# Optimization experiments

Hardware: AMD Instinct MI355X
Metric: run time of the kernel (lower is better)

## Reference

```python
import jax, jax.numpy as jnp
import numpy as np

B, T, D, H = 32, 2048, 256, 256  # batch, length, input_size, hidden_size


def _lstm_layer(x, W_ih, W_hh, b, reverse):
    """Single-direction LSTM over time. x: [B,T,Din]; W_ih: [4H,Din]; W_hh: [4H,H]; b: [4H].
    Gate order: i, f, g, o (PyTorch convention). Returns hidden states [B,T,H]."""
    # Precompute input contribution for all timesteps in one big GEMM.
    xg = jnp.einsum('btd,gd->btg', x, W_ih) + b  # [B,T,4H]
    Hh = W_hh.shape[1]
    Bb = x.shape[0]

    def step(carry, xg_t):
        h, c = carry
        g = xg_t + h @ W_hh.T  # [B,4H]
        i, f, gc, o = jnp.split(g, 4, axis=-1)
        c = jax.nn.sigmoid(f) * c + jax.nn.sigmoid(i) * jnp.tanh(gc)
        h = jax.nn.sigmoid(o) * jnp.tanh(c)
        return (h, c), h

    init = (jnp.zeros((Bb, Hh), x.dtype), jnp.zeros((Bb, Hh), x.dtype))
    _, hs = jax.lax.scan(step, init, jnp.swapaxes(xg, 0, 1), reverse=reverse)  # [T,B,H]
    return jnp.swapaxes(hs, 0, 1)  # [B,T,H]


def setup_inputs() -> dict:
    key = jax.random.key(0)
    ks = jax.random.split(key, 13)
    s = 0.05
    G = 4 * H
    inp = {
        'x': jax.random.normal(ks[0], (B, T, D), dtype=jnp.float32),
        # layer 0 (input size D), forward and reverse directions
        'W_ih_f0': jax.random.normal(ks[1], (G, D), dtype=jnp.float32) * s,
        'W_hh_f0': jax.random.normal(ks[2], (G, H), dtype=jnp.float32) * s,
        'b_f0': jnp.zeros((G,), dtype=jnp.float32),
        'W_ih_r0': jax.random.normal(ks[3], (G, D), dtype=jnp.float32) * s,
        'W_hh_r0': jax.random.normal(ks[4], (G, H), dtype=jnp.float32) * s,
        'b_r0': jnp.zeros((G,), dtype=jnp.float32),
        # layer 1 (input size 2H because bidirectional)
        'W_ih_f1': jax.random.normal(ks[5], (G, 2 * H), dtype=jnp.float32) * s,
        'W_hh_f1': jax.random.normal(ks[6], (G, H), dtype=jnp.float32) * s,
        'b_f1': jnp.zeros((G,), dtype=jnp.float32),
        'W_ih_r1': jax.random.normal(ks[7], (G, 2 * H), dtype=jnp.float32) * s,
        'W_hh_r1': jax.random.normal(ks[8], (G, H), dtype=jnp.float32) * s,
        'b_r1': jnp.zeros((G,), dtype=jnp.float32),
    }
    return inp


def reference(x, W_ih_f0, W_hh_f0, b_f0, W_ih_r0, W_hh_r0, b_r0,
              W_ih_f1, W_hh_f1, b_f1, W_ih_r1, W_hh_r1, b_r1):
    # Layer 0: bidirectional over raw input
    h0 = jnp.concatenate([
        _lstm_layer(x, W_ih_f0, W_hh_f0, b_f0, reverse=False),
        _lstm_layer(x, W_ih_r0, W_hh_r0, b_r0, reverse=True),
    ], axis=-1)  # [B,T,2H]
    # Layer 1: bidirectional over concatenated hidden states
    h1 = jnp.concatenate([
        _lstm_layer(h0, W_ih_f1, W_hh_f1, b_f1, reverse=False),
        _lstm_layer(h0, W_ih_r1, W_hh_r1, b_r1, reverse=True),
    ], axis=-1)  # [B,T,2H]
    return h1
```

## Files before the change

kernel.cpp:

```cpp
#include <hip/hip_runtime.h>
#include <stdint.h>


#define Bn 32
#define Tn 2048
#define Hn 256

#define L2E 1.4426950408889634f
#define L2E2 2.8853900817779268f
#define L2E4 5.7707801635558535f

typedef short short8 __attribute__((ext_vector_type(8)));
typedef float f32x4 __attribute__((ext_vector_type(4)));
typedef unsigned int u32x4 __attribute__((ext_vector_type(4)));

extern "C" __device__ float __ocml_native_exp2_f32(float);

__device__ inline unsigned short f2b(float f) {
  union { float f; unsigned u; } v; v.f = f;
  unsigned r = v.u + 0x7fffu + ((v.u >> 16) & 1u);
  return (unsigned short)(r >> 16);
}
__device__ inline float asf(unsigned u) {
  union { unsigned u; float f; } v; v.u = u; return v.f;
}
__device__ inline float sig2(float x) {
  return __builtin_amdgcn_rcpf(1.f + __ocml_native_exp2_f32(-x));
}

template <int K, bool AF32>
__global__ __launch_bounds__(256, 2) void xg_gemm(
    const void* __restrict__ Ain,
    const float* __restrict__ Wf, const float* __restrict__ bf_,
    const float* __restrict__ Wr, const float* __restrict__ br_,
    unsigned short* __restrict__ xg) {
  constexpr int KI = K / 32;
  const int bid = blockIdx.x;
  const int scan = bid & 1;
  const int sgrp = (bid >> 1) & 7;
  const int mchunk = bid >> 4;
  const int wave = threadIdx.x >> 6;
  const int lane = threadIdx.x & 63;
  const int l15 = lane & 15, quad = lane >> 4;
  const int stripe = sgrp * 4 + wave;
  const int gi0 = stripe * 32;
  const int wp = stripe & 7;
  const int gg = stripe >> 3;

  const float* W = scan ? Wr : Wf;
  const float* bias = scan ? br_ : bf_;
  const float gscale = (gg == 2) ? L2E2 : L2E;

  short8 bfr[KI][2];
  float bias2[2];
#pragma unroll
  for (int sub = 0; sub < 2; ++sub) {
    const int gi = gi0 + sub * 16 + l15;
    bias2[sub] = bias[gi] * gscale;
#pragma unroll
    for (int ki = 0; ki < KI; ++ki) {
      const float* src = W + (size_t)gi * K + ki * 32 + quad * 8;
      short8 v;
#pragma unroll
      for (int j = 0; j < 8; ++j) v[j] = (short)f2b(src[j] * gscale);
      bfr[ki][sub] = v;
    }
  }

  const size_t scanoff = (size_t)scan << 26;
#pragma unroll 1
  for (int mt0 = 0; mt0 < 16; ++mt0) {
    const int mt = mchunk * 16 + mt0;
    const size_t row = (size_t)mt * 16 + l15;
    f32x4 acc[2];
#pragma unroll
    for (int sub = 0; sub < 2; ++sub) {
      f32x4 bi = {bias2[sub], bias2[sub], bias2[sub], bias2[sub]};
      acc[sub] = bi;
    }
#pragma unroll
    for (int ki = 0; ki < KI; ++ki) {
      short8 af;
      if constexpr (AF32) {
        const float* ap = (const float*)Ain + row * K + ki * 32 + quad * 8;
        f32x4 a0 = *(const f32x4*)ap;
        f32x4 a1 = *(const f32x4*)(ap + 4);
#pragma unroll
        for (int j = 0; j < 4; ++j) { af[j] = (short)f2b(a0[j]); af[4 + j] = (short)f2b(a1[j]); }
      } else {
        const unsigned short* ap = (const unsigned short*)Ain + row * K + ki * 32 + quad * 8;
        af = *(const short8*)ap;
      }
#pragma unroll
      for (int sub = 0; sub < 2; ++sub)
        acc[sub] = __builtin_amdgcn_mfma_f32_16x16x32_bf16(af, bfr[ki][sub], acc[sub], 0, 0, 0);
    }
#pragma unroll
    for (int sub = 0; sub < 2; ++sub) {
#pragma unroll
      for (int r = 0; r < 4; ++r) {
        const int orow = mt * 16 + quad * 4 + r;
        const int m = orow >> 11, t = orow & 2047;
        size_t idx = scanoff
          + ((((size_t)t * 2 + (m >> 4)) * 8 + wp) << 11)
          + ((size_t)((((m >> 2) & 3) << 4) + l15) << 5)
          + (sub << 4) + (gg << 2) + (m & 3);
        xg[idx] = f2b(acc[sub][r]);
      }
    }
  }
}

template <bool LAYER1>
__global__ __launch_bounds__(512, 2) void lstm_scan(
    const unsigned short* __restrict__ xg,
    const float* __restrict__ Whh_f, const float* __restrict__ Whh_r,
    unsigned short* __restrict__ h0out,
    float* __restrict__ dout) {
  __shared__ __align__(16) char smem[131072 + 2 * 8192];

  const int bid = blockIdx.x;
  const int scan = bid & 1;
  const int mh = bid >> 1;
  const int wave = threadIdx.x >> 6;
  const int lane = threadIdx.x & 63;
  const int l15 = lane & 15, quad = lane >> 4;

  const float* Whh = scan ? Whh_r : Whh_f;

  short8 wres[2][3][8];
#pragma unroll
  for (int uh = 0; uh < 2; ++uh)
#pragma unroll
    for (int g = 0; g < 3; ++g) {
      const float ws = (g == 2) ? L2E2 : L2E;
#pragma unroll
      for (int ki = 0; ki < 8; ++ki) {
        const int col = g * 256 + wave * 32 + uh * 16 + l15;
        const float* src = Whh + ((size_t)col << 8) + ki * 32 + quad * 8;
        f32x4 a0 = *(const f32x4*)src;
        f32x4 a1 = *(const f32x4*)(src + 4);
        short8 v;
#pragma unroll
        for (int j = 0; j < 4; ++j) { v[j] = (short)f2b(a0[j] * ws); v[4 + j] = (short)f2b(a1[j] * ws); }
        wres[uh][g][ki] = v;
      }
    }
#pragma unroll
  for (int uh = 0; uh < 2; ++uh)
#pragma unroll
    for (int ki = 0; ki < 8; ++ki) {
      const int col = 768 + wave * 32 + uh * 16 + l15;
      const float* src = Whh + ((size_t)col << 8) + ki * 32 + quad * 8;
      f32x4 a0 = *(const f32x4*)src;
      f32x4 a1 = *(const f32x4*)(src + 4);
      short8 v;
#pragma unroll
      for (int j = 0; j < 4; ++j) { v[j] = (short)f2b(a0[j] * L2E); v[4 + j] = (short)f2b(a1[j] * L2E); }
      *(short8*)(smem + ((((wave << 1) + uh) << 3) + ki) * 1024 + lane * 16) = v;
    }

  const size_t scanoff = (size_t)scan << 26;
  const int tstep = scan ? -1 : 1;
  const int t0 = scan ? (Tn - 1) : 0;
  const size_t lane_off = (size_t)lane * 32;
  u32x4 xr[2][2];
  {
    const unsigned short* xb =
        xg + scanoff + ((((size_t)t0 * 2 + mh) * 8 + wave) << 11) + lane_off;
    xr[0][0] = *(const u32x4*)(xb + 0);
    xr[0][1] = *(const u32x4*)(xb + 8);
    xr[1][0] = *(const u32x4*)(xb + 16);
    xr[1][1] = *(const u32x4*)(xb + 24);
  }

  char* hbuf = smem + 131072;
  float c_st[2][4] = {{0.f, 0.f, 0.f, 0.f}, {0.f, 0.f, 0.f, 0.f}};

  __syncthreads();

#pragma unroll 1
  for (int s = 0; s < Tn; ++s) {
    const int t = scan ? (Tn - 1 - s) : s;
    const int tn = (s < Tn - 1) ? (t + tstep) : t;
    const unsigned short* xbn =
        xg + scanoff + ((((size_t)tn * 2 + mh) * 8 + wave) << 11) + lane_off;
    const int p_r = (s - 1) & 1, p_w = s & 1;

#pragma unroll
    for (int uh = 0; uh < 2; ++uh) {
      f32x4 acc[4];
#pragma unroll
      for (int g = 0; g < 4; ++g) {
        unsigned lo = xr[uh][g >> 1][2 * (g & 1)];
        unsigned hi = xr[uh][g >> 1][2 * (g & 1) + 1];
        acc[g][0] = asf(lo << 16); acc[g][1] = asf(lo & 0xffff0000u);
        acc[g][2] = asf(hi << 16); acc[g][3] = asf(hi & 0xffff0000u);
      }
      if (uh == 1) {
        xr[0][0] = *(const u32x4*)(xbn + 0);
        xr[0][1] = *(const u32x4*)(xbn + 8);
      }

      if (s > 0) {
        const char* hr = hbuf + p_r * 8192 + lane * 16;
        const char* wl0 = smem + (((wave << 1) + uh) << 13) + lane * 16;
#pragma unroll
        for (int ki = 0; ki < 8; ++ki) {
          short8 a = *(const short8*)(hr + (ki << 10));
          short8 wl = *(const short8*)(wl0 + (ki << 10));
          acc[0] = __builtin_amdgcn_mfma_f32_16x16x32_bf16(a, wres[uh][0][ki], acc[0], 0, 0, 0);
          acc[1] = __builtin_amdgcn_mfma_f32_16x16x32_bf16(a, wres[uh][1][ki], acc[1], 0, 0, 0);
          acc[2] = __builtin_amdgcn_mfma_f32_16x16x32_bf16(a, wres[uh][2][ki], acc[2], 0, 0, 0);
          acc[3] = __builtin_amdgcn_mfma_f32_16x16x32_bf16(a, wl,              acc[3], 0, 0, 0);
        }
      }

      const int ubase = wave * 32 + uh * 16 + l15;
      char* hwb = hbuf + p_w * 8192 + wave * 1024 +
                  ((uh * 2 + (l15 >> 3)) << 8) + (l15 & 7) * 2;
#pragma unroll
      for (int r = 0; r < 4; ++r) {
        float ig = sig2(acc[0][r]);
        float fg = sig2(acc[1][r]);
        float gt = __builtin_fmaf(sig2(acc[2][r]), L2E4, -L2E2);
        float og = sig2(acc[3][r]);
        float cv = __builtin_fmaf(fg, c_st[uh][r], ig * gt);
        c_st[uh][r] = cv;
        float hv = og * __builtin_fmaf(sig2(cv), 2.f, -1.f);
        unsigned short h16 = f2b(hv);
        int pk = __shfl_xor((int)h16, 1);
        const int row = quad * 4 + r;
        if (!(lane & 1)) {
          unsigned pv = (unsigned)h16 | ((unsigned)pk << 16);
          *(unsigned*)(hwb + row * 16) = pv;
        }
        const int b = mh * 16 + row;
        if constexpr (!LAYER1) {
          h0out[(((size_t)b * Tn + t) << 9) + scan * Hn + ubase] = h16;
        } else {
          dout[(((size_t)b * Tn + t) << 9) + scan * Hn + ubase] = hv;
        }
      }

      if (uh == 1) {
        xr[1][0] = *(const u32x4*)(xbn + 16);
        xr[1][1] = *(const u32x4*)(xbn + 24);
      }
    }

    __syncthreads();
  }
}

extern "C" void kernel_launch(void* const* d_in, const int* in_sizes, int n_in,
                              void* d_out, int out_size, void* d_ws, size_t ws_size,
                              hipStream_t stream) {
  (void)in_sizes; (void)n_in; (void)out_size; (void)ws_size;
  const float* x      = (const float*)d_in[0];
  const float* Wih_f0 = (const float*)d_in[1];
  const float* Whh_f0 = (const float*)d_in[2];
  const float* b_f0   = (const float*)d_in[3];
  const float* Wih_r0 = (const float*)d_in[4];
  const float* Whh_r0 = (const float*)d_in[5];
  const float* b_r0   = (const float*)d_in[6];
  const float* Wih_f1 = (const float*)d_in[7];
  const float* Whh_f1 = (const float*)d_in[8];
  const float* b_f1   = (const float*)d_in[9];
  const float* Wih_r1 = (const float*)d_in[10];
  const float* Whh_r1 = (const float*)d_in[11];
  const float* b_r1   = (const float*)d_in[12];

  char* ws = (char*)d_ws;
  unsigned short* xgbuf = (unsigned short*)ws;
  size_t off = (size_t)2 * Tn * Bn * 1024 * sizeof(unsigned short);
  unsigned short* h0out = (unsigned short*)(ws + off);

  dim3 blkA(256), blkB(512);
  xg_gemm<256, true><<<dim3(4096), blkA, 0, stream>>>(
      (const void*)x, Wih_f0, b_f0, Wih_r0, b_r0, xgbuf);
  lstm_scan<false><<<dim3(4), blkB, 0, stream>>>(
      xgbuf, Whh_f0, Whh_r0, h0out, (float*)nullptr);
  xg_gemm<512, false><<<dim3(4096), blkA, 0, stream>>>(
      (const void*)h0out, Wih_f1, b_f1, Wih_r1, b_r1, xgbuf);
  lstm_scan<true><<<dim3(4), blkB, 0, stream>>>(
      xgbuf, Whh_f1, Whh_r1, (unsigned short*)nullptr, (float*)d_out);
}
```

Measured before the change: 14.87 ms.

## Move g-gate recurrent weights to global scratch and merge gate transcendentals

The g-gate slice of W_hh moves out of registers into a per-block bf16 buffer in global memory (L2-resident). Both unit halves are computed in one MFMA loop, which frees registers and exposes more independent MFMA chains per step. The gate nonlinearities are rewritten to share reciprocals (rcp of products), cutting transcendental ops per element. Output stores are paired via shuffle, and __syncthreads is replaced by an explicit lgkmcnt wait plus barrier. The cost is extra global/L2 loads for the g weights on every time step of the serial recurrence.

Measured after the change: 20.13 ms. 1.35x slower.

```diff
diff --git a/kernel.cpp b/kernel.cpp
--- a/kernel.cpp
+++ b/kernel.cpp
@@ -8,7 +8,6 @@
 
 #define L2E 1.4426950408889634f
 #define L2E2 2.8853900817779268f
-#define L2E4 5.7707801635558535f
 
 typedef short short8 __attribute__((ext_vector_type(8)));
 typedef float f32x4 __attribute__((ext_vector_type(4)));
@@ -23,9 +22,6 @@
 }
 __device__ inline float asf(unsigned u) {
   union { unsigned u; float f; } v; v.u = u; return v.f;
-}
-__device__ inline float sig2(float x) {
-  return __builtin_amdgcn_rcpf(1.f + __ocml_native_exp2_f32(-x));
 }
 
 template <int K, bool AF32>
@@ -115,6 +111,7 @@
 __global__ __launch_bounds__(512, 2) void lstm_scan(
     const unsigned short* __restrict__ xg,
     const float* __restrict__ Whh_f, const float* __restrict__ Whh_r,
+    unsigned short* __restrict__ gw,
     unsigned short* __restrict__ h0out,
     float* __restrict__ dout) {
   __shared__ __align__(16) char smem[131072 + 2 * 8192];
@@ -128,12 +125,11 @@
 
   const float* Whh = scan ? Whh_r : Whh_f;
 
-  short8 wres[2][3][8];
+  short8 wres[2][2][8];
 #pragma unroll
   for (int uh = 0; uh < 2; ++uh)
 #pragma unroll
-    for (int g = 0; g < 3; ++g) {
-      const float ws = (g == 2) ? L2E2 : L2E;
+    for (int g = 0; g < 2; ++g)
 #pragma unroll
       for (int ki = 0; ki < 8; ++ki) {
         const int col = g * 256 + wave * 32 + uh * 16 + l15;
@@ -142,10 +138,9 @@
         f32x4 a1 = *(const f32x4*)(src + 4);
         short8 v;
 #pragma unroll
-        for (int j = 0; j < 4; ++j) { v[j] = (short)f2b(a0[j] * ws); v[4 + j] = (short)f2b(a1[j] * ws); }
+        for (int j = 0; j < 4; ++j) { v[j] = (short)f2b(a0[j] * L2E); v[4 + j] = (short)f2b(a1[j] * L2E); }
         wres[uh][g][ki] = v;
       }
-    }
 #pragma unroll
   for (int uh = 0; uh < 2; ++uh)
 #pragma unroll
@@ -158,6 +153,20 @@
 #pragma unroll
       for (int j = 0; j < 4; ++j) { v[j] = (short)f2b(a0[j] * L2E); v[4 + j] = (short)f2b(a1[j] * L2E); }
       *(short8*)(smem + ((((wave << 1) + uh) << 3) + ki) * 1024 + lane * 16) = v;
+    }
+  unsigned short* gws = gw + (size_t)bid * 65536;
+#pragma unroll
+  for (int uh = 0; uh < 2; ++uh)
+#pragma unroll
+    for (int ki = 0; ki < 8; ++ki) {
+      const int col = 512 + wave * 32 + uh * 16 + l15;
+      const float* src = Whh + ((size_t)col << 8) + ki * 32 + quad * 8;
+      f32x4 a0 = *(const f32x4*)src;
+      f32x4 a1 = *(const f32x4*)(src + 4);
+      short8 v;
+#pragma unroll
+      for (int j = 0; j < 4; ++j) { v[j] = (short)f2b(a0[j] * L2E2); v[4 + j] = (short)f2b(a1[j] * L2E2); }
+      *(short8*)(gws + ((((wave << 1) + uh) << 3) + ki) * 512 + lane * 8) = v;
     }
 
   const size_t scanoff = (size_t)scan << 26;
@@ -179,6 +188,8 @@
 
   __syncthreads();
 
+  const unsigned short* gwp = gws + (wave << 13) + lane * 8;
+
 #pragma unroll 1
   for (int s = 0; s < Tn; ++s) {
     const int t = scan ? (Tn - 1 - s) : s;
@@ -187,69 +198,82 @@
         xg + scanoff + ((((size_t)tn * 2 + mh) * 8 + wave) << 11) + lane_off;
     const int p_r = (s - 1) & 1, p_w = s & 1;
 
-#pragma unroll
-    for (int uh = 0; uh < 2; ++uh) {
-      f32x4 acc[4];
+    f32x4 acc[2][4];
+#pragma unroll
+    for (int uh = 0; uh < 2; ++uh)
 #pragma unroll
       for (int g = 0; g < 4; ++g) {
         unsigned lo = xr[uh][g >> 1][2 * (g & 1)];
         unsigned hi = xr[uh][g >> 1][2 * (g & 1) + 1];
-        acc[g][0] = asf(lo << 16); acc[g][1] = asf(lo & 0xffff0000u);
-        acc[g][2] = asf(hi << 16); acc[g][3] = asf(hi & 0xffff0000u);
-      }
-      if (uh == 1) {
-        xr[0][0] = *(const u32x4*)(xbn + 0);
-        xr[0][1] = *(const u32x4*)(xbn + 8);
-      }
-
-      if (s > 0) {
-        const char* hr = hbuf + p_r * 8192 + lane * 16;
-        const char* wl0 = smem + (((wave << 1) + uh) << 13) + lane * 16;
-#pragma unroll
-        for (int ki = 0; ki < 8; ++ki) {
-          short8 a = *(const short8*)(hr + (ki << 10));
-          short8 wl = *(const short8*)(wl0 + (ki << 10));
-          acc[0] = __builtin_amdgcn_mfma_f32_16x16x32_bf16(a, wres[uh][0][ki], acc[0], 0, 0, 0);
-          acc[1] = __builtin_amdgcn_mfma_f32_16x16x32_bf16(a, wres[uh][1][ki], acc[1], 0, 0, 0);
-          acc[2] = __builtin_amdgcn_mfma_f32_16x16x32_bf16(a, wres[uh][2][ki], acc[2], 0, 0, 0);
-          acc[3] = __builtin_amdgcn_mfma_f32_16x16x32_bf16(a, wl,              acc[3], 0, 0, 0);
-        }
-      }
-
+        acc[uh][g][0] = asf(lo << 16); acc[uh][g][1] = asf(lo & 0xffff0000u);
+        acc[uh][g][2] = asf(hi << 16); acc[uh][g][3] = asf(hi & 0xffff0000u);
+      }
+    xr[0][0] = *(const u32x4*)(xbn + 0);
+    xr[0][1] = *(const u32x4*)(xbn + 8);
+    xr[1][0] = *(const u32x4*)(xbn + 16);
+    xr[1][1] = *(const u32x4*)(xbn + 24);
+
+    if (s > 0) {
+      const char* hr = hbuf + p_r * 8192 + lane * 16;
+      const char* wlb = smem + (wave << 14) + lane * 16;
+#pragma unroll
+      for (int ki = 0; ki < 8; ++ki) {
+        short8 a = *(const short8*)(hr + (ki << 10));
+        short8 wl0 = *(const short8*)(wlb + (ki << 10));
+        short8 wl1 = *(const short8*)(wlb + 8192 + (ki << 10));
+        short8 g0 = *(const short8*)(gwp + (ki << 9));
+        short8 g1 = *(const short8*)(gwp + 4096 + (ki << 9));
+        acc[0][0] = __builtin_amdgcn_mfma_f32_16x16x32_bf16(a, wres[0][0][ki], acc[0][0], 0, 0, 0);
+        acc[0][1] = __builtin_amdgcn_mfma_f32_16x16x32_bf16(a, wres[0][1][ki], acc[0][1], 0, 0, 0);
+        acc[0][2] = __builtin_amdgcn_mfma_f32_16x16x32_bf16(a, g0,             acc[0][2], 0, 0, 0);
+        acc[0][3] = __builtin_amdgcn_mfma_f32_16x16x32_bf16(a, wl0,            acc[0][3], 0, 0, 0);
+        acc[1][0] = __builtin_amdgcn_mfma_f32_16x16x32_bf16(a, wres[1][0][ki], acc[1][0], 0, 0, 0);
+        acc[1][1] = __builtin_amdgcn_mfma_f32_16x16x32_bf16(a, wres[1][1][ki], acc[1][1], 0, 0, 0);
+        acc[1][2] = __builtin_amdgcn_mfma_f32_16x16x32_bf16(a, g1,             acc[1][2], 0, 0, 0);
+        acc[1][3] = __builtin_amdgcn_mfma_f32_16x16x32_bf16(a, wl1,            acc[1][3], 0, 0, 0);
+      }
+    }
+
+#pragma unroll
+    for (int uh = 0; uh < 2; ++uh) {
       const int ubase = wave * 32 + uh * 16 + l15;
       char* hwb = hbuf + p_w * 8192 + wave * 1024 +
                   ((uh * 2 + (l15 >> 3)) << 8) + (l15 & 7) * 2;
 #pragma unroll
       for (int r = 0; r < 4; ++r) {
-        float ig = sig2(acc[0][r]);
-        float fg = sig2(acc[1][r]);
-        float gt = __builtin_fmaf(sig2(acc[2][r]), L2E4, -L2E2);
-        float og = sig2(acc[3][r]);
-        float cv = __builtin_fmaf(fg, c_st[uh][r], ig * gt);
-        c_st[uh][r] = cv;
-        float hv = og * __builtin_fmaf(sig2(cv), 2.f, -1.f);
+        float e0 = __ocml_native_exp2_f32(-acc[uh][0][r]);
+        float e1 = __ocml_native_exp2_f32(-acc[uh][1][r]);
+        float e2 = __ocml_native_exp2_f32(-acc[uh][2][r]);
+        float e3 = __ocml_native_exp2_f32(-acc[uh][3][r]);
+        float a0 = 1.f + e0, a1 = 1.f + e1, a2 = 1.f + e2, a3 = 1.f + e3;
+        float r02 = __builtin_amdgcn_rcpf(a0 * a2);
+        float tig = __builtin_fmaf(e2, -L2E2, L2E2) * r02;
+        float rf = __builtin_amdgcn_rcpf(a1);
+        float cs = __builtin_fmaf(rf, c_st[uh][r], tig);
+        c_st[uh][r] = cs;
+        float e4 = __ocml_native_exp2_f32(-cs);
+        float a4 = 1.f + e4;
+        float r34 = __builtin_amdgcn_rcpf(a3 * a4);
+        float hv = (1.f - e4) * r34;
         unsigned short h16 = f2b(hv);
         int pk = __shfl_xor((int)h16, 1);
         const int row = quad * 4 + r;
-        if (!(lane & 1)) {
-          unsigned pv = (unsigned)h16 | ((unsigned)pk << 16);
-          *(unsigned*)(hwb + row * 16) = pv;
+        const unsigned pv = (unsigned)h16 | ((unsigned)pk << 16);
+        if (!(lane & 1)) *(unsigned*)(hwb + row * 16) = pv;
+        const int b = mh * 16 + row;
+        const size_t oidx = (((size_t)b * Tn + t) << 9) + scan * Hn + ubase;
+        if constexpr (!LAYER1) {
+          if (!(lane & 1)) *(unsigned*)(h0out + oidx) = pv;
+        } else {
+          float pkf = __shfl_xor(hv, 1);
+          if (!(lane & 1)) { float2 st = {hv, pkf}; *(float2*)(dout + oidx) = st; }
         }
-        const int b = mh * 16 + row;
-        if constexpr (!LAYER1) {
-          h0out[(((size_t)b * Tn + t) << 9) + scan * Hn + ubase] = h16;
-        } else {
-          dout[(((size_t)b * Tn + t) << 9) + scan * Hn + ubase] = hv;
-        }
-      }
-
-      if (uh == 1) {
-        xr[1][0] = *(const u32x4*)(xbn + 16);
-        xr[1][1] = *(const u32x4*)(xbn + 24);
-      }
-    }
-
-    __syncthreads();
+      }
+    }
+
+    asm volatile("s_waitcnt lgkmcnt(0)" ::: "memory");
+    __builtin_amdgcn_s_barrier();
+    __builtin_amdgcn_sched_barrier(0);
   }
 }
 
@@ -275,14 +299,16 @@
   unsigned short* xgbuf = (unsigned short*)ws;
   size_t off = (size_t)2 * Tn * Bn * 1024 * sizeof(unsigned short);
   unsigned short* h0out = (unsigned short*)(ws + off);
+  off += (size_t)Bn * Tn * 512 * sizeof(unsigned short);
+  unsigned short* gwbuf = (unsigned short*)(ws + off);
 
   dim3 blkA(256), blkB(512);
   xg_gemm<256, true><<<dim3(4096), blkA, 0, stream>>>(
       (const void*)x, Wih_f0, b_f0, Wih_r0, b_r0, xgbuf);
   lstm_scan<false><<<dim3(4), blkB, 0, stream>>>(
-      xgbuf, Whh_f0, Whh_r0, h0out, (float*)nullptr);
+      xgbuf, Whh_f0, Whh_r0, gwbuf, h0out, (float*)nullptr);
   xg_gemm<512, false><<<dim3(4096), blkA, 0, stream>>>(
       (const void*)h0out, Wih_f1, b_f1, Wih_r1, b_r1, xgbuf);
   lstm_scan<true><<<dim3(4), blkB, 0, stream>>>(
-      xgbuf, Whh_f1, Whh_r1, (unsigned short*)nullptr, (float*)d_out);
-}
+      xgbuf, Whh_f1, Whh_r1, gwbuf, (unsigned short*)nullptr, (float*)d_out);
+}
```

## Split each LSTM scan across two cooperating blocks with global-memory flag handoff

Applied to the files above, without the earlier changes.

The recurrent scan grid grows from 4 to 8 blocks. Each pair of blocks owns half of the hidden units and keeps all four gates' weights in registers instead of partly in LDS. Partner halves of h are exchanged every timestep through a global buffer, with per-block step flags polled by atomic loads. The gate math is also restructured to share reciprocals, and the xg layout is rewritten to match the new per-half ownership. The aim is to halve the per-step matmul and activation work per block, at the cost of a cross-CU spin-wait handoff each step whose latency may dominate.

Result: slower. 45.53 ms (+206.1%).

```diff
diff --git a/kernel.cpp b/kernel.cpp
--- a/kernel.cpp
+++ b/kernel.cpp
@@ -8,7 +8,6 @@
 
 #define L2E 1.4426950408889634f
 #define L2E2 2.8853900817779268f
-#define L2E4 5.7707801635558535f
 
 typedef short short8 __attribute__((ext_vector_type(8)));
 typedef float f32x4 __attribute__((ext_vector_type(4)));
@@ -23,9 +22,6 @@
 }
 __device__ inline float asf(unsigned u) {
   union { unsigned u; float f; } v; v.u = u; return v.f;
-}
-__device__ inline float sig2(float x) {
-  return __builtin_amdgcn_rcpf(1.f + __ocml_native_exp2_f32(-x));
 }
 
 template <int K, bool AF32>
@@ -44,7 +40,6 @@
   const int l15 = lane & 15, quad = lane >> 4;
   const int stripe = sgrp * 4 + wave;
   const int gi0 = stripe * 32;
-  const int wp = stripe & 7;
   const int gg = stripe >> 3;
 
   const float* W = scan ? Wr : Wf;
@@ -97,14 +92,16 @@
     }
 #pragma unroll
     for (int sub = 0; sub < 2; ++sub) {
+      const int G = stripe * 2 + sub;
+      const int g_s = G >> 4, half_s = (G >> 3) & 1, w_s = G & 7;
 #pragma unroll
       for (int r = 0; r < 4; ++r) {
         const int orow = mt * 16 + quad * 4 + r;
         const int m = orow >> 11, t = orow & 2047;
         size_t idx = scanoff
-          + ((((size_t)t * 2 + (m >> 4)) * 8 + wp) << 11)
-          + ((size_t)((((m >> 2) & 3) << 4) + l15) << 5)
-          + (sub << 4) + (gg << 2) + (m & 3);
+          + (((size_t)t * 2 + (m >> 4)) << 14)
+          + (half_s << 13) + (w_s << 10)
+          + (((m >> 2) & 3) << 8) + (l15 << 4) + (g_s << 2) + (m & 3);
         xg[idx] = f2b(acc[sub][r]);
       }
     }
@@ -115,67 +112,60 @@
 __global__ __launch_bounds__(512, 2) void lstm_scan(
     const unsigned short* __restrict__ xg,
     const float* __restrict__ Whh_f, const float* __restrict__ Whh_r,
+    unsigned short* __restrict__ hx,
+    int* __restrict__ flags,
     unsigned short* __restrict__ h0out,
     float* __restrict__ dout) {
-  __shared__ __align__(16) char smem[131072 + 2 * 8192];
+  __shared__ __align__(16) char smem[2 * 4096];
 
   const int bid = blockIdx.x;
   const int scan = bid & 1;
-  const int mh = bid >> 1;
+  const int mh = (bid >> 1) & 1;
+  const int half = bid >> 2;
   const int wave = threadIdx.x >> 6;
   const int lane = threadIdx.x & 63;
   const int l15 = lane & 15, quad = lane >> 4;
 
   const float* Whh = scan ? Whh_r : Whh_f;
 
-  short8 wres[2][3][8];
-#pragma unroll
-  for (int uh = 0; uh < 2; ++uh)
-#pragma unroll
-    for (int g = 0; g < 3; ++g) {
-      const float ws = (g == 2) ? L2E2 : L2E;
-#pragma unroll
-      for (int ki = 0; ki < 8; ++ki) {
-        const int col = g * 256 + wave * 32 + uh * 16 + l15;
-        const float* src = Whh + ((size_t)col << 8) + ki * 32 + quad * 8;
-        f32x4 a0 = *(const f32x4*)src;
-        f32x4 a1 = *(const f32x4*)(src + 4);
-        short8 v;
-#pragma unroll
-        for (int j = 0; j < 4; ++j) { v[j] = (short)f2b(a0[j] * ws); v[4 + j] = (short)f2b(a1[j] * ws); }
-        wres[uh][g][ki] = v;
-      }
-    }
-#pragma unroll
-  for (int uh = 0; uh < 2; ++uh)
+  short8 wres[4][8];
+#pragma unroll
+  for (int g = 0; g < 4; ++g) {
+    const float ws = (g == 2) ? L2E2 : L2E;
 #pragma unroll
     for (int ki = 0; ki < 8; ++ki) {
-      const int col = 768 + wave * 32 + uh * 16 + l15;
+      const int col = g * Hn + half * 128 + wave * 16 + l15;
       const float* src = Whh + ((size_t)col << 8) + ki * 32 + quad * 8;
-      f32x4 a0 = *(const f32x4*)src;
-      f32x4 a1 = *(const f32x4*)(src + 4);
+      f32x4 v0 = *(const f32x4*)src;
+      f32x4 v1 = *(const f32x4*)(src + 4);
       short8 v;
 #pragma unroll
-      for (int j = 0; j < 4; ++j) { v[j] = (short)f2b(a0[j] * L2E); v[4 + j] = (short)f2b(a1[j] * L2E); }
-      *(short8*)(smem + ((((wave << 1) + uh) << 3) + ki) * 1024 + lane * 16) = v;
-    }
+      for (int j = 0; j < 4; ++j) { v[j] = (short)f2b(v0[j] * ws); v[4 + j] = (short)f2b(v1[j] * ws); }
+      wres[g][ki] = v;
+    }
+  }
+
+  const int slot = (scan * 2 + mh) * 2 + half;
+  const int pslot = slot ^ 1;
+  unsigned short* hxw = hx + (size_t)slot * 4096;
+  const unsigned short* hxp = hx + (size_t)pslot * 4096;
+  int* myflag = flags + slot;
+  int* pflag = flags + pslot;
 
   const size_t scanoff = (size_t)scan << 26;
   const int tstep = scan ? -1 : 1;
   const int t0 = scan ? (Tn - 1) : 0;
-  const size_t lane_off = (size_t)lane * 32;
-  u32x4 xr[2][2];
+  const size_t xbase0 = scanoff + ((size_t)half << 13) + ((size_t)wave << 10) + (size_t)lane * 16;
+  u32x4 xr[2];
   {
-    const unsigned short* xb =
-        xg + scanoff + ((((size_t)t0 * 2 + mh) * 8 + wave) << 11) + lane_off;
-    xr[0][0] = *(const u32x4*)(xb + 0);
-    xr[0][1] = *(const u32x4*)(xb + 8);
-    xr[1][0] = *(const u32x4*)(xb + 16);
-    xr[1][1] = *(const u32x4*)(xb + 24);
-  }
-
-  char* hbuf = smem + 131072;
-  float c_st[2][4] = {{0.f, 0.f, 0.f, 0.f}, {0.f, 0.f, 0.f, 0.f}};
+    const unsigned short* xb = xg + xbase0 + (((size_t)t0 * 2 + mh) << 14);
+    xr[0] = *(const u32x4*)(xb + 0);
+    xr[1] = *(const u32x4*)(xb + 8);
+  }
+
+  float c_st[4] = {0.f, 0.f, 0.f, 0.f};
+  const int ob = half ? 4 : 0;
+  const int pb = half ? 0 : 4;
 
   __syncthreads();
 
@@ -183,73 +173,108 @@
   for (int s = 0; s < Tn; ++s) {
     const int t = scan ? (Tn - 1 - s) : s;
     const int tn = (s < Tn - 1) ? (t + tstep) : t;
-    const unsigned short* xbn =
-        xg + scanoff + ((((size_t)tn * 2 + mh) * 8 + wave) << 11) + lane_off;
     const int p_r = (s - 1) & 1, p_w = s & 1;
 
-#pragma unroll
-    for (int uh = 0; uh < 2; ++uh) {
-      f32x4 acc[4];
-#pragma unroll
-      for (int g = 0; g < 4; ++g) {
-        unsigned lo = xr[uh][g >> 1][2 * (g & 1)];
-        unsigned hi = xr[uh][g >> 1][2 * (g & 1) + 1];
-        acc[g][0] = asf(lo << 16); acc[g][1] = asf(lo & 0xffff0000u);
-        acc[g][2] = asf(hi << 16); acc[g][3] = asf(hi & 0xffff0000u);
-      }
-      if (uh == 1) {
-        xr[0][0] = *(const u32x4*)(xbn + 0);
-        xr[0][1] = *(const u32x4*)(xbn + 8);
-      }
-
-      if (s > 0) {
-        const char* hr = hbuf + p_r * 8192 + lane * 16;
-        const char* wl0 = smem + (((wave << 1) + uh) << 13) + lane * 16;
-#pragma unroll
-        for (int ki = 0; ki < 8; ++ki) {
-          short8 a = *(const short8*)(hr + (ki << 10));
-          short8 wl = *(const short8*)(wl0 + (ki << 10));
-          acc[0] = __builtin_amdgcn_mfma_f32_16x16x32_bf16(a, wres[uh][0][ki], acc[0], 0, 0, 0);
-          acc[1] = __builtin_amdgcn_mfma_f32_16x16x32_bf16(a, wres[uh][1][ki], acc[1], 0, 0, 0);
-          acc[2] = __builtin_amdgcn_mfma_f32_16x16x32_bf16(a, wres[uh][2][ki], acc[2], 0, 0, 0);
-          acc[3] = __builtin_amdgcn_mfma_f32_16x16x32_bf16(a, wl,              acc[3], 0, 0, 0);
-        }
-      }
-
-      const int ubase = wave * 32 + uh * 16 + l15;
-      char* hwb = hbuf + p_w * 8192 + wave * 1024 +
-                  ((uh * 2 + (l15 >> 3)) << 8) + (l15 & 7) * 2;
+    f32x4 acc[4];
+#pragma unroll
+    for (int g = 0; g < 4; ++g) {
 #pragma unroll
       for (int r = 0; r < 4; ++r) {
-        float ig = sig2(acc[0][r]);
-        float fg = sig2(acc[1][r]);
-        float gt = __builtin_fmaf(sig2(acc[2][r]), L2E4, -L2E2);
-        float og = sig2(acc[3][r]);
-        float cv = __builtin_fmaf(fg, c_st[uh][r], ig * gt);
-        c_st[uh][r] = cv;
-        float hv = og * __builtin_fmaf(sig2(cv), 2.f, -1.f);
-        unsigned short h16 = f2b(hv);
-        int pk = __shfl_xor((int)h16, 1);
-        const int row = quad * 4 + r;
-        if (!(lane & 1)) {
-          unsigned pv = (unsigned)h16 | ((unsigned)pk << 16);
-          *(unsigned*)(hwb + row * 16) = pv;
-        }
-        const int b = mh * 16 + row;
-        if constexpr (!LAYER1) {
-          h0out[(((size_t)b * Tn + t) << 9) + scan * Hn + ubase] = h16;
-        } else {
-          dout[(((size_t)b * Tn + t) << 9) + scan * Hn + ubase] = hv;
-        }
-      }
-
-      if (uh == 1) {
-        xr[1][0] = *(const u32x4*)(xbn + 16);
-        xr[1][1] = *(const u32x4*)(xbn + 24);
-      }
-    }
-
-    __syncthreads();
+        const int e = g * 4 + r;
+        const unsigned w32 = xr[e >> 3][(e >> 1) & 3];
+        acc[g][r] = (r & 1) ? asf(w32 & 0xffff0000u) : asf(w32 << 16);
+      }
+    }
+    {
+      const unsigned short* xbn = xg + xbase0 + (((size_t)tn * 2 + mh) << 14);
+      xr[0] = *(const u32x4*)(xbn + 0);
+      xr[1] = *(const u32x4*)(xbn + 8);
+    }
+
+    if (s > 0) {
+      const char* hr = smem + p_r * 4096;
+      short8 a_own[4];
+#pragma unroll
+      for (int kil = 0; kil < 4; ++kil) {
+        int byt = l15 * 256 + kil * 64 + quad * 16;
+        byt ^= (l15 & 7) << 4;
+        a_own[kil] = *(const short8*)(hr + byt);
+      }
+      for (;;) {
+        int v = __hip_atomic_load(pflag, __ATOMIC_RELAXED, __HIP_MEMORY_SCOPE_AGENT);
+        if (v >= s) break;
+        __builtin_amdgcn_s_sleep(1);
+      }
+      const unsigned long long* pq = (const unsigned long long*)(hxp + p_r * 2048);
+      unsigned long long q[4][2];
+#pragma unroll
+      for (int kil = 0; kil < 4; ++kil) {
+        const int ei = (l15 * 128 + kil * 32 + quad * 8) >> 2;
+        q[kil][0] = __hip_atomic_load(pq + ei, __ATOMIC_RELAXED, __HIP_MEMORY_SCOPE_AGENT);
+        q[kil][1] = __hip_atomic_load(pq + ei + 1, __ATOMIC_RELAXED, __HIP_MEMORY_SCOPE_AGENT);
+      }
+#pragma unroll
+      for (int kil = 0; kil < 4; ++kil) {
+        const short8 a = a_own[kil];
+        acc[0] = __builtin_amdgcn_mfma_f32_16x16x32_bf16(a, wres[0][ob + kil], acc[0], 0, 0, 0);
+        acc[1] = __builtin_amdgcn_mfma_f32_16x16x32_bf16(a, wres[1][ob + kil], acc[1], 0, 0, 0);
+        acc[2] = __builtin_amdgcn_mfma_f32_16x16x32_bf16(a, wres[2][ob + kil], acc[2], 0, 0, 0);
+        acc[3] = __builtin_amdgcn_mfma_f32_16x16x32_bf16(a, wres[3][ob + kil], acc[3], 0, 0, 0);
+      }
+#pragma unroll
+      for (int kil = 0; kil < 4; ++kil) {
+        union { unsigned long long qq[2]; short8 s8; } u;
+        u.qq[0] = q[kil][0]; u.qq[1] = q[kil][1];
+        const short8 a = u.s8;
+        acc[0] = __builtin_amdgcn_mfma_f32_16x16x32_bf16(a, wres[0][pb + kil], acc[0], 0, 0, 0);
+        acc[1] = __builtin_amdgcn_mfma_f32_16x16x32_bf16(a, wres[1][pb + kil], acc[1], 0, 0, 0);
+        acc[2] = __builtin_amdgcn_mfma_f32_16x16x32_bf16(a, wres[2][pb + kil], acc[2], 0, 0, 0);
+        acc[3] = __builtin_amdgcn_mfma_f32_16x16x32_bf16(a, wres[3][pb + kil], acc[3], 0, 0, 0);
+      }
+    }
+
+#pragma unroll
+    for (int r = 0; r < 4; ++r) {
+      float e0 = __ocml_native_exp2_f32(-acc[0][r]);
+      float e1 = __ocml_native_exp2_f32(-acc[1][r]);
+      float e2 = __ocml_native_exp2_f32(-acc[2][r]);
+      float e3 = __ocml_native_exp2_f32(-acc[3][r]);
+      float a0 = 1.f + e0, a1 = 1.f + e1, a2 = 1.f + e2, a3 = 1.f + e3;
+      float r02 = __builtin_amdgcn_rcpf(a0 * a2);
+      float tig = __builtin_fmaf(e2, -L2E2, L2E2) * r02;
+      float rf = __builtin_amdgcn_rcpf(a1);
+      float cs = __builtin_fmaf(rf, c_st[r], tig);
+      c_st[r] = cs;
+      float e4 = __ocml_native_exp2_f32(-cs);
+      float r34 = __builtin_amdgcn_rcpf(a3 * (1.f + e4));
+      float hv = (1.f - e4) * r34;
+      unsigned short h16 = f2b(hv);
+      int pk = __shfl_xor((int)h16, 1);
+      const int row = quad * 4 + r;
+      const int ul = (wave << 4) + l15;
+      const unsigned pv = (unsigned)h16 | ((unsigned)pk << 16);
+      if (!(lane & 1)) {
+        int lb = p_w * 4096 + row * 256 + ul * 2;
+        lb ^= (row & 7) << 4;
+        *(unsigned*)(smem + lb) = pv;
+        __hip_atomic_store((unsigned*)(hxw + p_w * 2048 + row * 128 + ul),
+                           pv, __ATOMIC_RELAXED, __HIP_MEMORY_SCOPE_AGENT);
+      }
+      const int b = mh * 16 + row;
+      const size_t oidx = (((size_t)b * Tn + t) << 9) + scan * Hn + half * 128 + ul;
+      if constexpr (!LAYER1) {
+        if (!(lane & 1)) *(unsigned*)(h0out + oidx) = pv;
+      } else {
+        float pkf = __shfl_xor(hv, 1);
+        if (!(lane & 1)) { float2 st = {hv, pkf}; *(float2*)(dout + oidx) = st; }
+      }
+    }
+
+    asm volatile("s_waitcnt vmcnt(0) lgkmcnt(0)" ::: "memory");
+    __builtin_amdgcn_s_barrier();
+    __builtin_amdgcn_sched_barrier(0);
+    if (threadIdx.x == 0)
+      __hip_atomic_store(myflag, s + 1, __ATOMIC_RELAXED, __HIP_MEMORY_SCOPE_AGENT);
   }
 }
 
@@ -275,14 +300,21 @@
   unsigned short* xgbuf = (unsigned short*)ws;
   size_t off = (size_t)2 * Tn * Bn * 1024 * sizeof(unsigned short);
   unsigned short* h0out = (unsigned short*)(ws + off);
+  off += (size_t)Bn * Tn * 512 * sizeof(unsigned short);
+  unsigned short* hxbuf = (unsigned short*)(ws + off);
+  off += 65536;
+  int* flagsA = (int*)(ws + off);
+  int* flagsB = flagsA + 8;
+
+  hipMemsetAsync(flagsA, 0, 64, stream);
 
   dim3 blkA(256), blkB(512);
   xg_gemm<256, true><<<dim3(4096), blkA, 0, stream>>>(
       (const void*)x, Wih_f0, b_f0, Wih_r0, b_r0, xgbuf);
-  lstm_scan<false><<<dim3(4), blkB, 0, stream>>>(
-      xgbuf, Whh_f0, Whh_r0, h0out, (float*)nullptr);
+  lstm_scan<false><<<dim3(8), blkB, 0, stream>>>(
+      xgbuf, Whh_f0, Whh_r0, hxbuf, flagsA, h0out, (float*)nullptr);
   xg_gemm<512, false><<<dim3(4096), blkA, 0, stream>>>(
       (const void*)h0out, Wih_f1, b_f1, Wih_r1, b_r1, xgbuf);
-  lstm_scan<true><<<dim3(4), blkB, 0, stream>>>(
-      xgbuf, Whh_f1, Whh_r1, (unsigned short*)nullptr, (float*)d_out);
-}
+  lstm_scan<true><<<dim3(8), blkB, 0, stream>>>(
+      xgbuf, Whh_f1, Whh_r1, hxbuf, flagsB, (unsigned short*)nullptr, (float*)d_out);
+}
```
